# Performance work log

Measured on AMD Instinct MI355X. Metric: run time of the kernel, lower is better.

Reference implementation:

```python
import jax, jax.numpy as jnp
import numpy as np

B, T, C, H, W = 1, 7, 128, 64, 64
IC = C // 2
MB = 256  # codebook size (hardcoded in source)


def setup_inputs() -> dict:
    key = jax.random.key(0)
    ks = jax.random.split(key, 15)
    rn = lambda k, s, sc=1.0: sc * jax.random.normal(k, s, dtype=jnp.float32)
    return {
        "x": rn(ks[0], (B, T, C, H, W)),
        "gn_gamma": 1.0 + rn(ks[1], (C,), 0.1),
        "gn_beta": rn(ks[2], (C,), 0.1),
        "g_w": rn(ks[3], (IC, C), 0.05), "g_b": rn(ks[4], (IC,), 0.05),
        "theta_w": rn(ks[5], (IC, C), 0.05), "theta_b": rn(ks[6], (IC,), 0.05),
        "phi_w": rn(ks[7], (IC, C), 0.05), "phi_b": rn(ks[8], (IC,), 0.05),
        "wz_w": rn(ks[9], (C, IC * 7), 0.05), "wz_b": rn(ks[10], (C,), 0.05),
        "wz1_w": rn(ks[11], (C, IC), 0.05), "wz1_b": rn(ks[12], (C,), 0.05),
        "mb": rn(ks[13], (IC, MB)),
        "std": 4.0 * jnp.ones((1,), jnp.float32),
    }


def _groupnorm(v, gamma, beta, groups=32, eps=1e-6):
    # v: (B_, C_, H_, W_)
    b_ = v.shape[0]
    vr = v.reshape(b_, groups, -1)
    mu = vr.mean(axis=-1, keepdims=True)
    var = vr.var(axis=-1, keepdims=True)
    vn = ((vr - mu) * jax.lax.rsqrt(var + eps)).reshape(v.shape)
    return vn * gamma[:, None, None] + beta[:, None, None]


def _conv1x1(v, w, b):
    # v: (B_, Cin, H, W), w: (Cout, Cin)
    return jnp.einsum('bchw,oc->bohw', v, w) + b[:, None, None]


def reference(x, gn_gamma, gn_beta, g_w, g_b, theta_w, theta_b, phi_w, phi_b,
              wz_w, wz_b, wz1_w, wz1_b, mb, std):
    b, t, c, h, w = x.shape
    ic = g_w.shape[0]
    n = h * w

    # distance matrix D[(i,j),(k,l)] = (j-l)^2 + (i-k)^2  (row-major flatten of (i,j))
    yy, xx = jnp.meshgrid(jnp.arange(h), jnp.arange(w), indexing='ij')
    yf = yy.reshape(-1).astype(x.dtype)
    xf = xx.reshape(-1).astype(x.dtype)
    D = (xf[:, None] - xf[None, :]) ** 2 + (yf[:, None] - yf[None, :]) ** 2  # (n, n)
    weight = jnp.exp(-0.5 * D / (std[0] * std[0]))  # (n, n)

    q = x[:, 3]  # (b, c, h, w)
    hn = _groupnorm(x.reshape(b * t, c, h, w), gn_gamma, gn_beta)
    qn = _groupnorm(q, gn_gamma, gn_beta)

    g_x = _conv1x1(hn, g_w, g_b).reshape(b, t, ic, n)
    theta_x = _conv1x1(hn, theta_w, theta_b).reshape(b, t, ic, n)
    phi = _conv1x1(qn, phi_w, phi_b).reshape(b, ic, n).transpose(0, 2, 1)  # (b, n, ic)

    def frame(_, tg):
        theta_t, g_t = tg  # each (b, ic, n)
        f = jnp.einsum('bnc,bcm->bnm', phi, theta_t)        # (b, n, n)
        fdc = jax.nn.softmax(f, axis=-1) * weight            # post-softmax reweight
        y = jnp.einsum('bnm,bcm->bnc', fdc, g_t)            # (b, n, ic)
        return None, y

    _, ys = jax.lax.scan(frame, None,
                         (theta_x.transpose(1, 0, 2, 3), g_x.transpose(1, 0, 2, 3)))
    # ys: (t, b, n, ic) -> (b, t*ic, h, w)
    corr = ys.transpose(1, 0, 3, 2).reshape(b, t * ic, h, w)
    W_y = _conv1x1(corr, wz_w, wz_b)

    # codebook memory attention
    f1 = jnp.einsum('bnc,ck->bnk', phi, mb) * (float(ic) ** -0.5)
    fdc1 = jax.nn.softmax(f1, axis=-1)
    y1 = jnp.einsum('bnk,ck->bnc', fdc1, mb)  # (b, n, ic)
    qloss = jnp.mean(jnp.abs(phi - y1))
    y1 = y1.transpose(0, 2, 1).reshape(b, ic, h, w)
    W_y1 = _conv1x1(y1, wz1_w, wz1_b)

    z = W_y + q + W_y1
    return z, qloss
```

## Files before the change

kernel.cpp:

```cpp
#include <hip/hip_runtime.h>
#include <hip/hip_bf16.h>

#define TT 7
#define CCH 128
#define ICH 64
#define NHW 4096
#define NSPLIT 4
#define MCHUNK (NHW/NSPLIT)

typedef __attribute__((ext_vector_type(8))) short short8;
typedef __attribute__((ext_vector_type(4))) short sshort4;
typedef __attribute__((ext_vector_type(4))) float floatx4;

#define LOG2E 1.44269504f

static __device__ __forceinline__ short f2bf(float f){
  __hip_bfloat16 h = __float2bfloat16(f);
  return *reinterpret_cast<short*>(&h);
}
static __device__ __forceinline__ float bf2f(short s){
  __hip_bfloat16 h = *reinterpret_cast<__hip_bfloat16*>(&s);
  return __bfloat162float(h);
}

__global__ __launch_bounds__(256) void k_precast(const float* __restrict__ x,
    __hip_bfloat16* __restrict__ xbf, float* __restrict__ sacc, float* __restrict__ s2acc){
  __shared__ short tile[64][66];
  int t = blockIdx.y, n0 = blockIdx.x*64, zh = blockIdx.z;
  int ln = threadIdx.x & 63, w = threadIdx.x >> 6;
  float sl[4] = {0.f,0.f,0.f,0.f}, s2l[4] = {0.f,0.f,0.f,0.f};
  #pragma unroll 4
  for (int ci = 0; ci < 16; ++ci){
    int cl = w*16 + ci;
    float v = x[((size_t)t*CCH + zh*64 + cl)*NHW + n0 + ln];
    tile[ln][cl] = f2bf(v);
    sl[ci>>2]  += v;
    s2l[ci>>2] += v*v;
  }
  #pragma unroll
  for (int off = 32; off; off >>= 1){
    #pragma unroll
    for (int g = 0; g < 4; ++g){
      sl[g]  += __shfl_xor(sl[g],  off);
      s2l[g] += __shfl_xor(s2l[g], off);
    }
  }
  if (ln == 0){
    #pragma unroll
    for (int g = 0; g < 4; ++g){
      atomicAdd(&sacc [t*32 + zh*16 + w*4 + g], sl[g]);
      atomicAdd(&s2acc[t*32 + zh*16 + w*4 + g], s2l[g]);
    }
  }
  __syncthreads();
  int row = threadIdx.x >> 2, seg = threadIdx.x & 3;
  short* dst = reinterpret_cast<short*>(xbf) + ((size_t)t*NHW + n0 + row)*CCH + zh*64 + seg*16;
  #pragma unroll
  for (int k = 0; k < 2; ++k){
    short8 v;
    #pragma unroll
    for (int j = 0; j < 8; ++j) v[j] = tile[row][seg*16 + k*8 + j];
    *reinterpret_cast<short8*>(dst + k*8) = v;
  }
}

__global__ __launch_bounds__(256) void k_setup(
    const float* __restrict__ gw, const float* __restrict__ gb,
    const float* __restrict__ thw, const float* __restrict__ thb,
    const float* __restrict__ phw, const float* __restrict__ phb,
    const float* __restrict__ gamma, const float* __restrict__ beta,
    const float* __restrict__ sacc, const float* __restrict__ s2acc,
    __hip_bfloat16* __restrict__ Wth, float* __restrict__ bth,
    __hip_bfloat16* __restrict__ Wg,  float* __restrict__ bg,
    __hip_bfloat16* __restrict__ Wphi, float* __restrict__ bphi,
    const float* __restrict__ wz, const float* __restrict__ wz1,
    const float* __restrict__ wz_b, const float* __restrict__ wz1_b,
    const float* __restrict__ mb,
    __hip_bfloat16* __restrict__ wzcat, float* __restrict__ biasz,
    __hip_bfloat16* __restrict__ mbT, __hip_bfloat16* __restrict__ mbbf){
  if (blockIdx.x < 240){
    int w = threadIdx.x >> 6, lane = threadIdx.x & 63;
    int oidx = blockIdx.x*4 + w;
    const float *W, *B; __hip_bfloat16 *Wf; float *bfo; int t, o;
    float scale = 1.f;
    if (oidx < 448){ t = oidx >> 6; o = oidx & 63; W = thw; B = thb; Wf = Wth + ((size_t)t*ICH + o)*CCH; bfo = bth + t*64 + o; scale = LOG2E; }
    else if (oidx < 896){ int j = oidx - 448; t = j >> 6; o = j & 63; W = gw; B = gb; Wf = Wg + ((size_t)t*ICH + o)*CCH; bfo = bg + t*64 + o; }
    else { t = 3; o = oidx - 896; W = phw; B = phb; Wf = Wphi + (size_t)o*CCH; bfo = bphi + o; }
    float bp = 0.f;
    #pragma unroll
    for (int h = 0; h < 2; ++h){
      int c = h*64 + lane;
      int g = c >> 2;
      float m  = sacc [t*32+g] * (1.f/16384.f);
      float vr = s2acc[t*32+g] * (1.f/16384.f) - m*m;
      float rs = rsqrtf(vr + 1e-6f);
      float a  = gamma[c]*rs;
      float wv = W[o*CCH + c];
      Wf[c] = __float2bfloat16(wv * a * scale);
      bp += wv * (beta[c] - m*a);
    }
    #pragma unroll
    for (int off = 32; off; off >>= 1) bp += __shfl_xor(bp, off);
    if (lane == 0) *bfo = (bp + B[o]) * scale;
  } else {
    int idx = (blockIdx.x - 240)*256 + threadIdx.x;
    #pragma unroll
    for (int k = 0; k < 2; ++k){
      int i = idx + k*32768;
      int o = i >> 9, kk = i & 511;
      float v = (kk < 448) ? wz[o*448 + kk] : wz1[o*64 + (kk-448)];
      wzcat[i] = __float2bfloat16(v);
    }
    if (idx < 128) biasz[idx] = wz_b[idx] + wz1_b[idx];
    if (idx < 64*256){
      int c = idx >> 8, j = idx & 255;
      float v = mb[idx];
      mbbf[idx] = __float2bfloat16(v);
      mbT[j*64 + c] = __float2bfloat16(v);
    }
  }
}

__global__ __launch_bounds__(256) void k_conv(const __hip_bfloat16* __restrict__ xbf,
    const __hip_bfloat16* __restrict__ Wth, const float* __restrict__ bth,
    const __hip_bfloat16* __restrict__ Wg,  const float* __restrict__ bg,
    const __hip_bfloat16* __restrict__ Wphi, const float* __restrict__ bphi,
    __hip_bfloat16* __restrict__ thetaT, __hip_bfloat16* __restrict__ g_nat,
    __hip_bfloat16* __restrict__ phi_bf){
  const int t = blockIdx.y, n0 = blockIdx.x*64;
  const int w = threadIdx.x >> 6, lane = threadIdx.x & 63;
  const int l15 = lane & 15, quad = lane >> 4;

  const short* xb = reinterpret_cast<const short*>(xbf) + ((size_t)t*NHW + n0)*CCH;
  short8 B[4][4];
  #pragma unroll
  for (int nt = 0; nt < 4; ++nt)
    #pragma unroll
    for (int kk = 0; kk < 4; ++kk)
      B[nt][kk] = *reinterpret_cast<const short8*>(xb + (size_t)(nt*16 + l15)*CCH + kk*32 + quad*8);

  {
    const short* aw = reinterpret_cast<const short*>(Wth) + ((size_t)t*ICH + w*16 + l15)*CCH + quad*8;
    short8 A[4];
    #pragma unroll
    for (int kk = 0; kk < 4; ++kk) A[kk] = *reinterpret_cast<const short8*>(aw + kk*32);
    float4 bv = *reinterpret_cast<const float4*>(bth + t*64 + w*16 + quad*4);
    #pragma unroll
    for (int nt = 0; nt < 4; ++nt){
      floatx4 acc = (floatx4){0.f,0.f,0.f,0.f};
      #pragma unroll
      for (int kk = 0; kk < 4; ++kk) acc = __builtin_amdgcn_mfma_f32_16x16x32_bf16(A[kk], B[nt][kk], acc, 0, 0, 0);
      sshort4 pk;
      pk[0] = f2bf(acc[0] + bv.x); pk[1] = f2bf(acc[1] + bv.y);
      pk[2] = f2bf(acc[2] + bv.z); pk[3] = f2bf(acc[3] + bv.w);
      short* dst = reinterpret_cast<short*>(thetaT) + ((size_t)t*NHW + n0 + nt*16 + l15)*ICH + w*16 + quad*4;
      *reinterpret_cast<sshort4*>(dst) = pk;
    }
  }
  {
    const short* aw = reinterpret_cast<const short*>(Wg) + ((size_t)t*ICH + w*16 + l15)*CCH + quad*8;
    short8 A[4];
    #pragma unroll
    for (int kk = 0; kk < 4; ++kk) A[kk] = *reinterpret_cast<const short8*>(aw + kk*32);
    float4 bv = *reinterpret_cast<const float4*>(bg + t*64 + w*16 + quad*4);
    #pragma unroll
    for (int nt = 0; nt < 4; ++nt){
      floatx4 acc = (floatx4){0.f,0.f,0.f,0.f};
      #pragma unroll
      for (int kk = 0; kk < 4; ++kk) acc = __builtin_amdgcn_mfma_f32_16x16x32_bf16(A[kk], B[nt][kk], acc, 0, 0, 0);
      short* gb = reinterpret_cast<short*>(g_nat);
      float bvv[4] = {bv.x, bv.y, bv.z, bv.w};
      #pragma unroll
      for (int r = 0; r < 4; ++r)
        gb[((size_t)t*ICH + w*16 + quad*4 + r)*NHW + n0 + nt*16 + l15] = f2bf(acc[r] + bvv[r]);
    }
  }
  if (t == 3){
    const short* aw = reinterpret_cast<const short*>(Wphi) + (size_t)(w*16 + l15)*CCH + quad*8;
    short8 A[4];
    #pragma unroll
    for (int kk = 0; kk < 4; ++kk) A[kk] = *reinterpret_cast<const short8*>(aw + kk*32);
    float4 bv = *reinterpret_cast<const float4*>(bphi + w*16 + quad*4);
    #pragma unroll
    for (int nt = 0; nt < 4; ++nt){
      floatx4 acc = (floatx4){0.f,0.f,0.f,0.f};
      #pragma unroll
      for (int kk = 0; kk < 4; ++kk) acc = __builtin_amdgcn_mfma_f32_16x16x32_bf16(A[kk], B[nt][kk], acc, 0, 0, 0);
      sshort4 pk;
      pk[0] = f2bf(acc[0] + bv.x); pk[1] = f2bf(acc[1] + bv.y);
      pk[2] = f2bf(acc[2] + bv.z); pk[3] = f2bf(acc[3] + bv.w);
      short* dst = reinterpret_cast<short*>(phi_bf) + (size_t)(n0 + nt*16 + l15)*ICH + w*16 + quad*4;
      *reinterpret_cast<sshort4*>(dst) = pk;
    }
  }
}

__global__ __launch_bounds__(256, 4) void k_attn(
    const __hip_bfloat16* __restrict__ phi_bf,
    const __hip_bfloat16* __restrict__ thetaT,
    const __hip_bfloat16* __restrict__ g_nat,
    const float* __restrict__ stdp,
    float* __restrict__ Opart, float* __restrict__ Zpart)
{
  const int t    = blockIdx.z;
  const int sp   = blockIdx.y;
  const int w    = threadIdx.x >> 6;
  const int lane = threadIdx.x & 63;
  const int l15  = lane & 15;
  const int quad = lane >> 4;
  const int n0   = blockIdx.x*64;
  const int yn   = blockIdx.x;

  __shared__ short Plds[2][64][72];
  __shared__ float Zsh[4][64];

  const float sstd  = stdp[0];
  const float coefL = -0.5f / (sstd*sstd) * LOG2E;

  const short* phi_s = reinterpret_cast<const short*>(phi_bf);
  const short* th_s  = reinterpret_cast<const short*>(thetaT) + (size_t)t*NHW*ICH;
  const short* g_s   = reinterpret_cast<const short*>(g_nat)  + (size_t)t*ICH*NHW;

  short8 phB[4][2];
  #pragma unroll
  for (int nt = 0; nt < 4; ++nt){
    const short* pp = phi_s + (size_t)(n0 + nt*16 + l15)*ICH + quad*8;
    phB[nt][0] = *reinterpret_cast<const short8*>(pp);
    phB[nt][1] = *reinterpret_cast<const short8*>(pp + 32);
  }

  float wxv[4][4];
  {
    const int xm = w*16 + quad*4;
    #pragma unroll
    for (int nt = 0; nt < 4; ++nt){
      int xn = nt*16 + l15;
      #pragma unroll
      for (int r = 0; r < 4; ++r){
        int dx = xn - (xm + r);
        wxv[nt][r] = exp2f(coefL * (float)(dx*dx));
      }
    }
  }

  const int ci = w >> 1, nj = w & 1;
  floatx4 oacc[2][2];
  #pragma unroll
  for (int a = 0; a < 2; ++a)
    #pragma unroll
    for (int b = 0; b < 2; ++b) oacc[a][b] = (floatx4){0.f,0.f,0.f,0.f};
  float psum[4] = {0.f,0.f,0.f,0.f};

  int m0 = sp*MCHUNK;
  for (int it = 0; it < MCHUNK/64; ++it, m0 += 64){
    const int buf = it & 1;

    short8 gA[2][2];
    #pragma unroll
    for (int ct = 0; ct < 2; ++ct){
      const short* gp = g_s + (size_t)(ci*32 + ct*16 + l15)*NHW + m0 + quad*8;
      gA[ct][0] = *reinterpret_cast<const short8*>(gp);
      gA[ct][1] = *reinterpret_cast<const short8*>(gp + 32);
    }

    const short* tp = th_s + (size_t)(m0 + w*16 + l15)*ICH + quad*8;
    short8 a0 = *reinterpret_cast<const short8*>(tp);
    short8 a1 = *reinterpret_cast<const short8*>(tp + 32);

    floatx4 s[4];
    #pragma unroll
    for (int nt = 0; nt < 4; ++nt){
      floatx4 acc = (floatx4){0.f,0.f,0.f,0.f};
      acc = __builtin_amdgcn_mfma_f32_16x16x32_bf16(a0, phB[nt][0], acc, 0, 0, 0);
      s[nt] = __builtin_amdgcn_mfma_f32_16x16x32_bf16(a1, phB[nt][1], acc, 0, 0, 0);
    }

    const int ym = m0 >> 6;
    const int dy = yn - ym;
    const float wyv = exp2f(coefL * (float)(dy*dy));
    #pragma unroll
    for (int nt = 0; nt < 4; ++nt){
      float pw[4];
      #pragma unroll
      for (int r = 0; r < 4; ++r){
        float p = exp2f(s[nt][r]);
        psum[nt] += p;
        pw[r] = p * (wyv * wxv[nt][r]);
      }
      __hip_bfloat162 lo = __float22bfloat162_rn(make_float2(pw[0], pw[1]));
      __hip_bfloat162 hi = __float22bfloat162_rn(make_float2(pw[2], pw[3]));
      uint2 u;
      u.x = *reinterpret_cast<unsigned*>(&lo);
      u.y = *reinterpret_cast<unsigned*>(&hi);
      *reinterpret_cast<uint2*>(&Plds[buf][nt*16 + l15][w*16 + quad*4]) = u;
    }

    __syncthreads();

    short8 pB[2][2];
    #pragma unroll
    for (int nt2 = 0; nt2 < 2; ++nt2){
      const short* pr = &Plds[buf][nj*32 + nt2*16 + l15][quad*8];
      pB[nt2][0] = *reinterpret_cast<const short8*>(pr);
      pB[nt2][1] = *reinterpret_cast<const short8*>(pr + 32);
    }

    #pragma unroll
    for (int ct = 0; ct < 2; ++ct)
      #pragma unroll
      for (int nt2 = 0; nt2 < 2; ++nt2){
        oacc[ct][nt2] = __builtin_amdgcn_mfma_f32_16x16x32_bf16(gA[ct][0], pB[nt2][0], oacc[ct][nt2], 0, 0, 0);
        oacc[ct][nt2] = __builtin_amdgcn_mfma_f32_16x16x32_bf16(gA[ct][1], pB[nt2][1], oacc[ct][nt2], 0, 0, 0);
      }
  }

  float* Ob = Opart + (size_t)(t*NSPLIT + sp)*ICH*NHW;
  #pragma unroll
  for (int ct = 0; ct < 2; ++ct)
    #pragma unroll
    for (int nt2 = 0; nt2 < 2; ++nt2){
      int c = ci*32 + ct*16 + quad*4;
      int n = n0 + nj*32 + nt2*16 + l15;
      #pragma unroll
      for (int r = 0; r < 4; ++r)
        Ob[(size_t)(c + r)*NHW + n] = oacc[ct][nt2][r];
    }

  #pragma unroll
  for (int nt = 0; nt < 4; ++nt){
    float z = psum[nt];
    z += __shfl_xor(z, 16);
    z += __shfl_xor(z, 32);
    psum[nt] = z;
  }
  if (quad == 0){
    #pragma unroll
    for (int nt = 0; nt < 4; ++nt) Zsh[w][nt*16 + l15] = psum[nt];
  }
  __syncthreads();
  if (threadIdx.x < 64){
    float z = Zsh[0][threadIdx.x] + Zsh[1][threadIdx.x] + Zsh[2][threadIdx.x] + Zsh[3][threadIdx.x];
    Zpart[(size_t)(t*NSPLIT + sp)*NHW + n0 + threadIdx.x] = z;
  }
}

__global__ __launch_bounds__(256) void k_merge(const float* __restrict__ Opart,
    const float* __restrict__ Zpart, __hip_bfloat16* __restrict__ corrT){
  __shared__ short tile[64][72];
  __shared__ float zinv[64];
  const int t = blockIdx.y, n0 = blockIdx.x*64;

  if (threadIdx.x < 64){
    float zs = 0.f;
    #pragma unroll
    for (int s = 0; s < NSPLIT; ++s)
      zs += Zpart[(size_t)(t*NSPLIT + s)*NHW + n0 + threadIdx.x];
    zinv[threadIdx.x] = 1.f / zs;
  }
  __syncthreads();

  const int nq = threadIdx.x & 15, cc = threadIdx.x >> 4;
  #pragma unroll
  for (int cp = 0; cp < 4; ++cp){
    int c = cp*16 + cc;
    float4 acc = {0.f,0.f,0.f,0.f};
    #pragma unroll
    for (int s = 0; s < NSPLIT; ++s){
      float4 v = *reinterpret_cast<const float4*>(
        Opart + ((size_t)(t*NSPLIT + s)*ICH + c)*NHW + n0 + nq*4);
      acc.x += v.x; acc.y += v.y; acc.z += v.z; acc.w += v.w;
    }
    tile[nq*4+0][c] = f2bf(acc.x * zinv[nq*4+0]);
    tile[nq*4+1][c] = f2bf(acc.y * zinv[nq*4+1]);
    tile[nq*4+2][c] = f2bf(acc.z * zinv[nq*4+2]);
    tile[nq*4+3][c] = f2bf(acc.w * zinv[nq*4+3]);
  }
  __syncthreads();

  #pragma unroll
  for (int rep = 0; rep < 2; ++rep){
    int idx = rep*256 + threadIdx.x;
    int n = idx >> 3, seg = idx & 7;
    short8 v = *reinterpret_cast<short8*>(&tile[n][seg*8]);
    *reinterpret_cast<short8*>(reinterpret_cast<short*>(corrT)
        + (size_t)(n0 + n)*512 + t*64 + seg*8) = v;
  }
}

__global__ __launch_bounds__(256) void k_mb(const __hip_bfloat16* __restrict__ phi_bf,
    const __hip_bfloat16* __restrict__ mbT, const __hip_bfloat16* __restrict__ mbbf,
    __hip_bfloat16* __restrict__ corrT, float* __restrict__ qacc){
  const int n0 = blockIdx.x*32;
  const int w = threadIdx.x >> 6, lane = threadIdx.x & 63;
  const int l15 = lane & 15, quad = lane >> 4;

  __shared__ short P[32][264];
  __shared__ float Zsh[4][32];

  const short* phi_s = reinterpret_cast<const short*>(phi_bf);
  const short* mbT_s = reinterpret_cast<const short*>(mbT);
  const short* mb_s  = reinterpret_cast<const short*>(mbbf);

  short8 Bp[2][2];
  #pragma unroll
  for (int nt = 0; nt < 2; ++nt){
    const short* pp = phi_s + (size_t)(n0 + nt*16 + l15)*ICH + quad*8;
    Bp[nt][0] = *reinterpret_cast<const short8*>(pp);
    Bp[nt][1] = *reinterpret_cast<const short8*>(pp + 32);
  }
  float psum[2] = {0.f, 0.f};
  #pragma unroll
  for (int jt = 0; jt < 4; ++jt){
    const short* ap = mbT_s + (size_t)(w*64 + jt*16 + l15)*64 + quad*8;
    short8 A0 = *reinterpret_cast<const short8*>(ap);
    short8 A1 = *reinterpret_cast<const short8*>(ap + 32);
    #pragma unroll
    for (int nt = 0; nt < 2; ++nt){
      floatx4 acc = (floatx4){0.f,0.f,0.f,0.f};
      acc = __builtin_amdgcn_mfma_f32_16x16x32_bf16(A0, Bp[nt][0], acc, 0, 0, 0);
      acc = __builtin_amdgcn_mfma_f32_16x16x32_bf16(A1, Bp[nt][1], acc, 0, 0, 0);
      sshort4 pk;
      #pragma unroll
      for (int r = 0; r < 4; ++r){
        float p = exp2f(acc[r] * (0.125f*LOG2E));
        psum[nt] += p;
        pk[r] = f2bf(p);
      }
      *reinterpret_cast<sshort4*>(&P[nt*16 + l15][w*64 + jt*16 + quad*4]) = pk;
    }
  }
  #pragma unroll
  for (int nt = 0; nt < 2; ++nt){
    float z = psum[nt];
    z += __shfl_xor(z, 16);
    z += __shfl_xor(z, 32);
    if (quad == 0) Zsh[w][nt*16 + l15] = z;
  }
  __syncthreads();

  float ql = 0.f;
  #pragma unroll
  for (int nt = 0; nt < 2; ++nt){
    floatx4 acc = (floatx4){0.f,0.f,0.f,0.f};
    #pragma unroll
    for (int kk = 0; kk < 8; ++kk){
      const short* ap = mb_s + (size_t)(w*16 + l15)*256 + kk*32 + quad*8;
      short8 A = *reinterpret_cast<const short8*>(ap);
      short8 B = *reinterpret_cast<const short8*>(&P[nt*16 + l15][kk*32 + quad*8]);
      acc = __builtin_amdgcn_mfma_f32_16x16x32_bf16(A, B, acc, 0, 0, 0);
    }
    int nn = nt*16 + l15;
    float zt = Zsh[0][nn] + Zsh[1][nn] + Zsh[2][nn] + Zsh[3][nn];
    float rz = 1.f / zt;
    const short* ph = phi_s + (size_t)(n0 + nn)*ICH + w*16 + quad*4;
    sshort4 ph4 = *reinterpret_cast<const sshort4*>(ph);
    sshort4 pk;
    #pragma unroll
    for (int r = 0; r < 4; ++r){
      float y = acc[r] * rz;
      ql += fabsf(bf2f(ph4[r]) - y);
      pk[r] = f2bf(y);
    }
    short* dst = reinterpret_cast<short*>(corrT) + (size_t)(n0 + nn)*512 + 448 + w*16 + quad*4;
    *reinterpret_cast<sshort4*>(dst) = pk;
  }
  #pragma unroll
  for (int off = 32; off; off >>= 1) ql += __shfl_xor(ql, off);
  if (lane == 0) atomicAdd(qacc, ql);
}

__global__ __launch_bounds__(256) void k_z(const __hip_bfloat16* __restrict__ corrT,
    const __hip_bfloat16* __restrict__ wzcat, const float* __restrict__ biasz,
    const float* __restrict__ x, const float* __restrict__ qacc,
    float* __restrict__ out){
  const int n0 = blockIdx.x*16;
  const int w = threadIdx.x >> 6, lane = threadIdx.x & 63;
  const int l15 = lane & 15, quad = lane >> 4;
  const int o0 = blockIdx.y*64 + w*16;

  const short* ct_s = reinterpret_cast<const short*>(corrT) + (size_t)(n0 + l15)*512 + quad*8;
  const short* wz_s = reinterpret_cast<const short*>(wzcat) + (size_t)(o0 + l15)*512 + quad*8;

  floatx4 acc = (floatx4){0.f,0.f,0.f,0.f};
  #pragma unroll
  for (int kk = 0; kk < 16; ++kk){
    short8 A = *reinterpret_cast<const short8*>(wz_s + kk*32);
    short8 B = *reinterpret_cast<const short8*>(ct_s + kk*32);
    acc = __builtin_amdgcn_mfma_f32_16x16x32_bf16(A, B, acc, 0, 0, 0);
  }
  float4 bz = *reinterpret_cast<const float4*>(biasz + o0 + quad*4);
  float bzv[4] = {bz.x, bz.y, bz.z, bz.w};
  #pragma unroll
  for (int r = 0; r < 4; ++r){
    int o = o0 + quad*4 + r;
    int n = n0 + l15;
    float q = x[((size_t)3*CCH + o)*NHW + n];
    out[(size_t)o*NHW + n] = acc[r] + bzv[r] + q;
  }
  if (blockIdx.x == 0 && blockIdx.y == 0 && threadIdx.x == 0)
    out[(size_t)CCH*NHW] = qacc[0] * (1.f/262144.f);
}

extern "C" void kernel_launch(void* const* d_in, const int* in_sizes, int n_in,
                              void* d_out, int out_size, void* d_ws, size_t ws_size,
                              hipStream_t stream){
  const float* x     = (const float*)d_in[0];
  const float* gamma = (const float*)d_in[1];
  const float* beta  = (const float*)d_in[2];
  const float* g_w   = (const float*)d_in[3];
  const float* g_b   = (const float*)d_in[4];
  const float* th_w  = (const float*)d_in[5];
  const float* th_b  = (const float*)d_in[6];
  const float* ph_w  = (const float*)d_in[7];
  const float* ph_b  = (const float*)d_in[8];
  const float* wz_w  = (const float*)d_in[9];
  const float* wz_b  = (const float*)d_in[10];
  const float* wz1_w = (const float*)d_in[11];
  const float* wz1_b = (const float*)d_in[12];
  const float* mb    = (const float*)d_in[13];
  const float* stdp  = (const float*)d_in[14];
  float* out = (float*)d_out;

  char* ws = (char*)d_ws;
  size_t off = 0;
  auto alloc = [&](size_t bytes)->char*{
    char* p = ws + off; off += (bytes + 255) & ~(size_t)255; return p;
  };
  float* zbuf    = (float*)alloc(452*4);
  float* sacc    = zbuf;
  float* s2acc   = zbuf + 224;
  float* qacc    = zbuf + 448;
  __hip_bfloat16* xbf    = (__hip_bfloat16*)alloc((size_t)TT*NHW*CCH*2);
  __hip_bfloat16* Wth    = (__hip_bfloat16*)alloc((size_t)TT*ICH*CCH*2);
  float* bth             = (float*)alloc(TT*64*4);
  __hip_bfloat16* Wg     = (__hip_bfloat16*)alloc((size_t)TT*ICH*CCH*2);
  float* bg              = (float*)alloc(TT*64*4);
  __hip_bfloat16* Wphi   = (__hip_bfloat16*)alloc((size_t)ICH*CCH*2);
  float* bphi            = (float*)alloc(64*4);
  __hip_bfloat16* wzcat  = (__hip_bfloat16*)alloc((size_t)128*512*2);
  float* biasz           = (float*)alloc(128*4);
  __hip_bfloat16* mbT    = (__hip_bfloat16*)alloc((size_t)256*64*2);
  __hip_bfloat16* mbbf   = (__hip_bfloat16*)alloc((size_t)64*256*2);
  __hip_bfloat16* thetaT = (__hip_bfloat16*)alloc((size_t)TT*NHW*ICH*2);
  __hip_bfloat16* g_nat  = (__hip_bfloat16*)alloc((size_t)TT*NHW*ICH*2);
  __hip_bfloat16* phi_bf = (__hip_bfloat16*)alloc((size_t)NHW*ICH*2);
  __hip_bfloat16* corrT  = (__hip_bfloat16*)alloc((size_t)NHW*512*2);
  float* Opart   = (float*)alloc((size_t)TT*NSPLIT*ICH*NHW*4);
  float* Zpart   = (float*)alloc((size_t)TT*NSPLIT*NHW*4);

  hipMemsetAsync(zbuf, 0, 452*4, stream);
  k_precast<<<dim3(64,7,2), 256, 0, stream>>>(x, xbf, sacc, s2acc);
  k_setup<<<368, 256, 0, stream>>>(g_w, g_b, th_w, th_b, ph_w, ph_b, gamma, beta,
                                   sacc, s2acc, Wth, bth, Wg, bg, Wphi, bphi,
                                   wz_w, wz1_w, wz_b, wz1_b, mb, wzcat, biasz, mbT, mbbf);
  k_conv<<<dim3(64,7), 256, 0, stream>>>(xbf, Wth, bth, Wg, bg, Wphi, bphi,
                                         thetaT, g_nat, phi_bf);
  k_attn<<<dim3(64,NSPLIT,7), 256, 0, stream>>>(phi_bf, thetaT, g_nat, stdp, Opart, Zpart);
  k_merge<<<dim3(64,7), 256, 0, stream>>>(Opart, Zpart, corrT);
  k_mb  <<<128, 256, 0, stream>>>(phi_bf, mbT, mbbf, corrT, qacc);
  k_z   <<<dim3(256,2), 256, 0, stream>>>(corrT, wzcat, biasz, x, qacc, out);
}
```

Measured before the change: 247.1 us.

## Drop memset and atomics, split conv into two jobs, merge merge+mb kernels

Group-norm statistics and the qloss sum are now written as per-block partial sums and reduced deterministically by the consumer kernels, replacing the atomics. This also removes the memset launch. The conv kernel gets a z dimension so theta/phi and g projections run in separate blocks, doubling parallelism. The merge and codebook kernels are fused into one launch, and k_attn's launch bounds are raised to 5 waves. Fewer launches and more blocks are traded for serial reduction loops in k_setup and k_z and possible register pressure in k_attn.

```diff
diff --git a/kernel.cpp b/kernel.cpp
--- a/kernel.cpp
+++ b/kernel.cpp
@@ -24,7 +24,7 @@
 }
 
 __global__ __launch_bounds__(256) void k_precast(const float* __restrict__ x,
-    __hip_bfloat16* __restrict__ xbf, float* __restrict__ sacc, float* __restrict__ s2acc){
+    __hip_bfloat16* __restrict__ xbf, float* __restrict__ spart, float* __restrict__ spart2){
   __shared__ short tile[64][66];
   int t = blockIdx.y, n0 = blockIdx.x*64, zh = blockIdx.z;
   int ln = threadIdx.x & 63, w = threadIdx.x >> 6;
@@ -46,11 +46,10 @@
     }
   }
   if (ln == 0){
-    #pragma unroll
-    for (int g = 0; g < 4; ++g){
-      atomicAdd(&sacc [t*32 + zh*16 + w*4 + g], sl[g]);
-      atomicAdd(&s2acc[t*32 + zh*16 + w*4 + g], s2l[g]);
-    }
+    float* sp  = spart  + (size_t)blockIdx.x*224 + t*32 + zh*16 + w*4;
+    float* sp2 = spart2 + (size_t)blockIdx.x*224 + t*32 + zh*16 + w*4;
+    #pragma unroll
+    for (int g = 0; g < 4; ++g){ sp[g] = sl[g]; sp2[g] = s2l[g]; }
   }
   __syncthreads();
   int row = threadIdx.x >> 2, seg = threadIdx.x & 3;
@@ -69,7 +68,7 @@
     const float* __restrict__ thw, const float* __restrict__ thb,
     const float* __restrict__ phw, const float* __restrict__ phb,
     const float* __restrict__ gamma, const float* __restrict__ beta,
-    const float* __restrict__ sacc, const float* __restrict__ s2acc,
+    const float* __restrict__ spart, const float* __restrict__ spart2,
     __hip_bfloat16* __restrict__ Wth, float* __restrict__ bth,
     __hip_bfloat16* __restrict__ Wg,  float* __restrict__ bg,
     __hip_bfloat16* __restrict__ Wphi, float* __restrict__ bphi,
@@ -86,18 +85,28 @@
     if (oidx < 448){ t = oidx >> 6; o = oidx & 63; W = thw; B = thb; Wf = Wth + ((size_t)t*ICH + o)*CCH; bfo = bth + t*64 + o; scale = LOG2E; }
     else if (oidx < 896){ int j = oidx - 448; t = j >> 6; o = j & 63; W = gw; B = gb; Wf = Wg + ((size_t)t*ICH + o)*CCH; bfo = bg + t*64 + o; }
     else { t = 3; o = oidx - 896; W = phw; B = phb; Wf = Wphi + (size_t)o*CCH; bfo = bphi + o; }
+    float mv[2], rv[2];
+    #pragma unroll
+    for (int h = 0; h < 2; ++h){
+      int gid = t*32 + ((h*64 + lane) >> 2);
+      float S = 0.f, S2 = 0.f;
+      for (int i = 0; i < 64; ++i){
+        S  += spart [(size_t)i*224 + gid];
+        S2 += spart2[(size_t)i*224 + gid];
+      }
+      float m  = S * (1.f/16384.f);
+      float vr = S2 * (1.f/16384.f) - m*m;
+      mv[h] = m;
+      rv[h] = rsqrtf(vr + 1e-6f);
+    }
     float bp = 0.f;
     #pragma unroll
     for (int h = 0; h < 2; ++h){
       int c = h*64 + lane;
-      int g = c >> 2;
-      float m  = sacc [t*32+g] * (1.f/16384.f);
-      float vr = s2acc[t*32+g] * (1.f/16384.f) - m*m;
-      float rs = rsqrtf(vr + 1e-6f);
-      float a  = gamma[c]*rs;
+      float a  = gamma[c]*rv[h];
       float wv = W[o*CCH + c];
       Wf[c] = __float2bfloat16(wv * a * scale);
-      bp += wv * (beta[c] - m*a);
+      bp += wv * (beta[c] - mv[h]*a);
     }
     #pragma unroll
     for (int off = 32; off; off >>= 1) bp += __shfl_xor(bp, off);
@@ -127,7 +136,7 @@
     const __hip_bfloat16* __restrict__ Wphi, const float* __restrict__ bphi,
     __hip_bfloat16* __restrict__ thetaT, __hip_bfloat16* __restrict__ g_nat,
     __hip_bfloat16* __restrict__ phi_bf){
-  const int t = blockIdx.y, n0 = blockIdx.x*64;
+  const int t = blockIdx.y, n0 = blockIdx.x*64, job = blockIdx.z;
   const int w = threadIdx.x >> 6, lane = threadIdx.x & 63;
   const int l15 = lane & 15, quad = lane >> 4;
 
@@ -139,25 +148,44 @@
     for (int kk = 0; kk < 4; ++kk)
       B[nt][kk] = *reinterpret_cast<const short8*>(xb + (size_t)(nt*16 + l15)*CCH + kk*32 + quad*8);
 
-  {
-    const short* aw = reinterpret_cast<const short*>(Wth) + ((size_t)t*ICH + w*16 + l15)*CCH + quad*8;
-    short8 A[4];
-    #pragma unroll
-    for (int kk = 0; kk < 4; ++kk) A[kk] = *reinterpret_cast<const short8*>(aw + kk*32);
-    float4 bv = *reinterpret_cast<const float4*>(bth + t*64 + w*16 + quad*4);
-    #pragma unroll
-    for (int nt = 0; nt < 4; ++nt){
-      floatx4 acc = (floatx4){0.f,0.f,0.f,0.f};
-      #pragma unroll
-      for (int kk = 0; kk < 4; ++kk) acc = __builtin_amdgcn_mfma_f32_16x16x32_bf16(A[kk], B[nt][kk], acc, 0, 0, 0);
-      sshort4 pk;
-      pk[0] = f2bf(acc[0] + bv.x); pk[1] = f2bf(acc[1] + bv.y);
-      pk[2] = f2bf(acc[2] + bv.z); pk[3] = f2bf(acc[3] + bv.w);
-      short* dst = reinterpret_cast<short*>(thetaT) + ((size_t)t*NHW + n0 + nt*16 + l15)*ICH + w*16 + quad*4;
-      *reinterpret_cast<sshort4*>(dst) = pk;
-    }
-  }
-  {
+  if (job == 0){
+    {
+      const short* aw = reinterpret_cast<const short*>(Wth) + ((size_t)t*ICH + w*16 + l15)*CCH + quad*8;
+      short8 A[4];
+      #pragma unroll
+      for (int kk = 0; kk < 4; ++kk) A[kk] = *reinterpret_cast<const short8*>(aw + kk*32);
+      float4 bv = *reinterpret_cast<const float4*>(bth + t*64 + w*16 + quad*4);
+      #pragma unroll
+      for (int nt = 0; nt < 4; ++nt){
+        floatx4 acc = (floatx4){0.f,0.f,0.f,0.f};
+        #pragma unroll
+        for (int kk = 0; kk < 4; ++kk) acc = __builtin_amdgcn_mfma_f32_16x16x32_bf16(A[kk], B[nt][kk], acc, 0, 0, 0);
+        sshort4 pk;
+        pk[0] = f2bf(acc[0] + bv.x); pk[1] = f2bf(acc[1] + bv.y);
+        pk[2] = f2bf(acc[2] + bv.z); pk[3] = f2bf(acc[3] + bv.w);
+        short* dst = reinterpret_cast<short*>(thetaT) + ((size_t)t*NHW + n0 + nt*16 + l15)*ICH + w*16 + quad*4;
+        *reinterpret_cast<sshort4*>(dst) = pk;
+      }
+    }
+    if (t == 3){
+      const short* aw = reinterpret_cast<const short*>(Wphi) + (size_t)(w*16 + l15)*CCH + quad*8;
+      short8 A[4];
+      #pragma unroll
+      for (int kk = 0; kk < 4; ++kk) A[kk] = *reinterpret_cast<const short8*>(aw + kk*32);
+      float4 bv = *reinterpret_cast<const float4*>(bphi + w*16 + quad*4);
+      #pragma unroll
+      for (int nt = 0; nt < 4; ++nt){
+        floatx4 acc = (floatx4){0.f,0.f,0.f,0.f};
+        #pragma unroll
+        for (int kk = 0; kk < 4; ++kk) acc = __builtin_amdgcn_mfma_f32_16x16x32_bf16(A[kk], B[nt][kk], acc, 0, 0, 0);
+        sshort4 pk;
+        pk[0] = f2bf(acc[0] + bv.x); pk[1] = f2bf(acc[1] + bv.y);
+        pk[2] = f2bf(acc[2] + bv.z); pk[3] = f2bf(acc[3] + bv.w);
+        short* dst = reinterpret_cast<short*>(phi_bf) + (size_t)(n0 + nt*16 + l15)*ICH + w*16 + quad*4;
+        *reinterpret_cast<sshort4*>(dst) = pk;
+      }
+    }
+  } else {
     const short* aw = reinterpret_cast<const short*>(Wg) + ((size_t)t*ICH + w*16 + l15)*CCH + quad*8;
     short8 A[4];
     #pragma unroll
@@ -175,27 +203,9 @@
         gb[((size_t)t*ICH + w*16 + quad*4 + r)*NHW + n0 + nt*16 + l15] = f2bf(acc[r] + bvv[r]);
     }
   }
-  if (t == 3){
-    const short* aw = reinterpret_cast<const short*>(Wphi) + (size_t)(w*16 + l15)*CCH + quad*8;
-    short8 A[4];
-    #pragma unroll
-    for (int kk = 0; kk < 4; ++kk) A[kk] = *reinterpret_cast<const short8*>(aw + kk*32);
-    float4 bv = *reinterpret_cast<const float4*>(bphi + w*16 + quad*4);
-    #pragma unroll
-    for (int nt = 0; nt < 4; ++nt){
-      floatx4 acc = (floatx4){0.f,0.f,0.f,0.f};
-      #pragma unroll
-      for (int kk = 0; kk < 4; ++kk) acc = __builtin_amdgcn_mfma_f32_16x16x32_bf16(A[kk], B[nt][kk], acc, 0, 0, 0);
-      sshort4 pk;
-      pk[0] = f2bf(acc[0] + bv.x); pk[1] = f2bf(acc[1] + bv.y);
-      pk[2] = f2bf(acc[2] + bv.z); pk[3] = f2bf(acc[3] + bv.w);
-      short* dst = reinterpret_cast<short*>(phi_bf) + (size_t)(n0 + nt*16 + l15)*ICH + w*16 + quad*4;
-      *reinterpret_cast<sshort4*>(dst) = pk;
-    }
-  }
-}
-
-__global__ __launch_bounds__(256, 4) void k_attn(
+}
+
+__global__ __launch_bounds__(256, 5) void k_attn(
     const __hip_bfloat16* __restrict__ phi_bf,
     const __hip_bfloat16* __restrict__ thetaT,
     const __hip_bfloat16* __restrict__ g_nat,
@@ -344,134 +354,140 @@
   }
 }
 
-__global__ __launch_bounds__(256) void k_merge(const float* __restrict__ Opart,
-    const float* __restrict__ Zpart, __hip_bfloat16* __restrict__ corrT){
+__global__ __launch_bounds__(256) void k_post(const float* __restrict__ Opart,
+    const float* __restrict__ Zpart,
+    const __hip_bfloat16* __restrict__ phi_bf,
+    const __hip_bfloat16* __restrict__ mbT, const __hip_bfloat16* __restrict__ mbbf,
+    __hip_bfloat16* __restrict__ corrT, float* __restrict__ qpart){
   __shared__ short tile[64][72];
   __shared__ float zinv[64];
-  const int t = blockIdx.y, n0 = blockIdx.x*64;
-
-  if (threadIdx.x < 64){
-    float zs = 0.f;
-    #pragma unroll
-    for (int s = 0; s < NSPLIT; ++s)
-      zs += Zpart[(size_t)(t*NSPLIT + s)*NHW + n0 + threadIdx.x];
-    zinv[threadIdx.x] = 1.f / zs;
-  }
-  __syncthreads();
-
-  const int nq = threadIdx.x & 15, cc = threadIdx.x >> 4;
-  #pragma unroll
-  for (int cp = 0; cp < 4; ++cp){
-    int c = cp*16 + cc;
-    float4 acc = {0.f,0.f,0.f,0.f};
-    #pragma unroll
-    for (int s = 0; s < NSPLIT; ++s){
-      float4 v = *reinterpret_cast<const float4*>(
-        Opart + ((size_t)(t*NSPLIT + s)*ICH + c)*NHW + n0 + nq*4);
-      acc.x += v.x; acc.y += v.y; acc.z += v.z; acc.w += v.w;
-    }
-    tile[nq*4+0][c] = f2bf(acc.x * zinv[nq*4+0]);
-    tile[nq*4+1][c] = f2bf(acc.y * zinv[nq*4+1]);
-    tile[nq*4+2][c] = f2bf(acc.z * zinv[nq*4+2]);
-    tile[nq*4+3][c] = f2bf(acc.w * zinv[nq*4+3]);
-  }
-  __syncthreads();
-
-  #pragma unroll
-  for (int rep = 0; rep < 2; ++rep){
-    int idx = rep*256 + threadIdx.x;
-    int n = idx >> 3, seg = idx & 7;
-    short8 v = *reinterpret_cast<short8*>(&tile[n][seg*8]);
-    *reinterpret_cast<short8*>(reinterpret_cast<short*>(corrT)
-        + (size_t)(n0 + n)*512 + t*64 + seg*8) = v;
-  }
-}
-
-__global__ __launch_bounds__(256) void k_mb(const __hip_bfloat16* __restrict__ phi_bf,
-    const __hip_bfloat16* __restrict__ mbT, const __hip_bfloat16* __restrict__ mbbf,
-    __hip_bfloat16* __restrict__ corrT, float* __restrict__ qacc){
-  const int n0 = blockIdx.x*32;
-  const int w = threadIdx.x >> 6, lane = threadIdx.x & 63;
-  const int l15 = lane & 15, quad = lane >> 4;
-
   __shared__ short P[32][264];
   __shared__ float Zsh[4][32];
-
-  const short* phi_s = reinterpret_cast<const short*>(phi_bf);
-  const short* mbT_s = reinterpret_cast<const short*>(mbT);
-  const short* mb_s  = reinterpret_cast<const short*>(mbbf);
-
-  short8 Bp[2][2];
-  #pragma unroll
-  for (int nt = 0; nt < 2; ++nt){
-    const short* pp = phi_s + (size_t)(n0 + nt*16 + l15)*ICH + quad*8;
-    Bp[nt][0] = *reinterpret_cast<const short8*>(pp);
-    Bp[nt][1] = *reinterpret_cast<const short8*>(pp + 32);
-  }
-  float psum[2] = {0.f, 0.f};
-  #pragma unroll
-  for (int jt = 0; jt < 4; ++jt){
-    const short* ap = mbT_s + (size_t)(w*64 + jt*16 + l15)*64 + quad*8;
-    short8 A0 = *reinterpret_cast<const short8*>(ap);
-    short8 A1 = *reinterpret_cast<const short8*>(ap + 32);
+  __shared__ float qred[4];
+
+  const int b = blockIdx.x;
+  if (b < 448){
+    const int t = b >> 6, n0 = (b & 63)*64;
+    if (threadIdx.x < 64){
+      float zs = 0.f;
+      #pragma unroll
+      for (int s = 0; s < NSPLIT; ++s)
+        zs += Zpart[(size_t)(t*NSPLIT + s)*NHW + n0 + threadIdx.x];
+      zinv[threadIdx.x] = 1.f / zs;
+    }
+    __syncthreads();
+
+    const int nq = threadIdx.x & 15, cc = threadIdx.x >> 4;
+    #pragma unroll
+    for (int cp = 0; cp < 4; ++cp){
+      int c = cp*16 + cc;
+      float4 acc = {0.f,0.f,0.f,0.f};
+      #pragma unroll
+      for (int s = 0; s < NSPLIT; ++s){
+        float4 v = *reinterpret_cast<const float4*>(
+          Opart + ((size_t)(t*NSPLIT + s)*ICH + c)*NHW + n0 + nq*4);
+        acc.x += v.x; acc.y += v.y; acc.z += v.z; acc.w += v.w;
+      }
+      tile[nq*4+0][c] = f2bf(acc.x * zinv[nq*4+0]);
+      tile[nq*4+1][c] = f2bf(acc.y * zinv[nq*4+1]);
+      tile[nq*4+2][c] = f2bf(acc.z * zinv[nq*4+2]);
+      tile[nq*4+3][c] = f2bf(acc.w * zinv[nq*4+3]);
+    }
+    __syncthreads();
+
+    #pragma unroll
+    for (int rep = 0; rep < 2; ++rep){
+      int idx = rep*256 + threadIdx.x;
+      int n = idx >> 3, seg = idx & 7;
+      short8 v = *reinterpret_cast<short8*>(&tile[n][seg*8]);
+      *reinterpret_cast<short8*>(reinterpret_cast<short*>(corrT)
+          + (size_t)(n0 + n)*512 + t*64 + seg*8) = v;
+    }
+  } else {
+    const int mbid = b - 448;
+    const int n0 = mbid*32;
+    const int w = threadIdx.x >> 6, lane = threadIdx.x & 63;
+    const int l15 = lane & 15, quad = lane >> 4;
+
+    const short* phi_s = reinterpret_cast<const short*>(phi_bf);
+    const short* mbT_s = reinterpret_cast<const short*>(mbT);
+    const short* mb_s  = reinterpret_cast<const short*>(mbbf);
+
+    short8 Bp[2][2];
+    #pragma unroll
+    for (int nt = 0; nt < 2; ++nt){
+      const short* pp = phi_s + (size_t)(n0 + nt*16 + l15)*ICH + quad*8;
+      Bp[nt][0] = *reinterpret_cast<const short8*>(pp);
+      Bp[nt][1] = *reinterpret_cast<const short8*>(pp + 32);
+    }
+    float psum[2] = {0.f, 0.f};
+    #pragma unroll
+    for (int jt = 0; jt < 4; ++jt){
+      const short* ap = mbT_s + (size_t)(w*64 + jt*16 + l15)*64 + quad*8;
+      short8 A0 = *reinterpret_cast<const short8*>(ap);
+      short8 A1 = *reinterpret_cast<const short8*>(ap + 32);
+      #pragma unroll
+      for (int nt = 0; nt < 2; ++nt){
+        floatx4 acc = (floatx4){0.f,0.f,0.f,0.f};
+        acc = __builtin_amdgcn_mfma_f32_16x16x32_bf16(A0, Bp[nt][0], acc, 0, 0, 0);
+        acc = __builtin_amdgcn_mfma_f32_16x16x32_bf16(A1, Bp[nt][1], acc, 0, 0, 0);
+        sshort4 pk;
+        #pragma unroll
+        for (int r = 0; r < 4; ++r){
+          float p = exp2f(acc[r] * (0.125f*LOG2E));
+          psum[nt] += p;
+          pk[r] = f2bf(p);
+        }
+        *reinterpret_cast<sshort4*>(&P[nt*16 + l15][w*64 + jt*16 + quad*4]) = pk;
+      }
+    }
+    #pragma unroll
+    for (int nt = 0; nt < 2; ++nt){
+      float z = psum[nt];
+      z += __shfl_xor(z, 16);
+      z += __shfl_xor(z, 32);
+      if (quad == 0) Zsh[w][nt*16 + l15] = z;
+    }
+    __syncthreads();
+
+    float ql = 0.f;
     #pragma unroll
     for (int nt = 0; nt < 2; ++nt){
       floatx4 acc = (floatx4){0.f,0.f,0.f,0.f};
-      acc = __builtin_amdgcn_mfma_f32_16x16x32_bf16(A0, Bp[nt][0], acc, 0, 0, 0);
-      acc = __builtin_amdgcn_mfma_f32_16x16x32_bf16(A1, Bp[nt][1], acc, 0, 0, 0);
+      #pragma unroll
+      for (int kk = 0; kk < 8; ++kk){
+        const short* ap = mb_s + (size_t)(w*16 + l15)*256 + kk*32 + quad*8;
+        short8 A = *reinterpret_cast<const short8*>(ap);
+        short8 Bv = *reinterpret_cast<const short8*>(&P[nt*16 + l15][kk*32 + quad*8]);
+        acc = __builtin_amdgcn_mfma_f32_16x16x32_bf16(A, Bv, acc, 0, 0, 0);
+      }
+      int nn = nt*16 + l15;
+      float zt = Zsh[0][nn] + Zsh[1][nn] + Zsh[2][nn] + Zsh[3][nn];
+      float rz = 1.f / zt;
+      const short* ph = phi_s + (size_t)(n0 + nn)*ICH + w*16 + quad*4;
+      sshort4 ph4 = *reinterpret_cast<const sshort4*>(ph);
       sshort4 pk;
       #pragma unroll
       for (int r = 0; r < 4; ++r){
-        float p = exp2f(acc[r] * (0.125f*LOG2E));
-        psum[nt] += p;
-        pk[r] = f2bf(p);
-      }
-      *reinterpret_cast<sshort4*>(&P[nt*16 + l15][w*64 + jt*16 + quad*4]) = pk;
-    }
-  }
-  #pragma unroll
-  for (int nt = 0; nt < 2; ++nt){
-    float z = psum[nt];
-    z += __shfl_xor(z, 16);
-    z += __shfl_xor(z, 32);
-    if (quad == 0) Zsh[w][nt*16 + l15] = z;
-  }
-  __syncthreads();
-
-  float ql = 0.f;
-  #pragma unroll
-  for (int nt = 0; nt < 2; ++nt){
-    floatx4 acc = (floatx4){0.f,0.f,0.f,0.f};
-    #pragma unroll
-    for (int kk = 0; kk < 8; ++kk){
-      const short* ap = mb_s + (size_t)(w*16 + l15)*256 + kk*32 + quad*8;
-      short8 A = *reinterpret_cast<const short8*>(ap);
-      short8 B = *reinterpret_cast<const short8*>(&P[nt*16 + l15][kk*32 + quad*8]);
-      acc = __builtin_amdgcn_mfma_f32_16x16x32_bf16(A, B, acc, 0, 0, 0);
-    }
-    int nn = nt*16 + l15;
-    float zt = Zsh[0][nn] + Zsh[1][nn] + Zsh[2][nn] + Zsh[3][nn];
-    float rz = 1.f / zt;
-    const short* ph = phi_s + (size_t)(n0 + nn)*ICH + w*16 + quad*4;
-    sshort4 ph4 = *reinterpret_cast<const sshort4*>(ph);
-    sshort4 pk;
-    #pragma unroll
-    for (int r = 0; r < 4; ++r){
-      float y = acc[r] * rz;
-      ql += fabsf(bf2f(ph4[r]) - y);
-      pk[r] = f2bf(y);
-    }
-    short* dst = reinterpret_cast<short*>(corrT) + (size_t)(n0 + nn)*512 + 448 + w*16 + quad*4;
-    *reinterpret_cast<sshort4*>(dst) = pk;
-  }
-  #pragma unroll
-  for (int off = 32; off; off >>= 1) ql += __shfl_xor(ql, off);
-  if (lane == 0) atomicAdd(qacc, ql);
+        float y = acc[r] * rz;
+        ql += fabsf(bf2f(ph4[r]) - y);
+        pk[r] = f2bf(y);
+      }
+      short* dst = reinterpret_cast<short*>(corrT) + (size_t)(n0 + nn)*512 + 448 + w*16 + quad*4;
+      *reinterpret_cast<sshort4*>(dst) = pk;
+    }
+    #pragma unroll
+    for (int off = 32; off; off >>= 1) ql += __shfl_xor(ql, off);
+    if (lane == 0) qred[w] = ql;
+    __syncthreads();
+    if (threadIdx.x == 0)
+      qpart[mbid] = qred[0] + qred[1] + qred[2] + qred[3];
+  }
 }
 
 __global__ __launch_bounds__(256) void k_z(const __hip_bfloat16* __restrict__ corrT,
     const __hip_bfloat16* __restrict__ wzcat, const float* __restrict__ biasz,
-    const float* __restrict__ x, const float* __restrict__ qacc,
+    const float* __restrict__ x, const float* __restrict__ qpart,
     float* __restrict__ out){
   const int n0 = blockIdx.x*16;
   const int w = threadIdx.x >> 6, lane = threadIdx.x & 63;
@@ -497,8 +513,11 @@
     float q = x[((size_t)3*CCH + o)*NHW + n];
     out[(size_t)o*NHW + n] = acc[r] + bzv[r] + q;
   }
-  if (blockIdx.x == 0 && blockIdx.y == 0 && threadIdx.x == 0)
-    out[(size_t)CCH*NHW] = qacc[0] * (1.f/262144.f);
+  if (blockIdx.x == 0 && blockIdx.y == 0 && threadIdx.x == 0){
+    float s = 0.f;
+    for (int i = 0; i < 128; ++i) s += qpart[i];
+    out[(size_t)CCH*NHW] = s * (1.f/262144.f);
+  }
 }
 
 extern "C" void kernel_launch(void* const* d_in, const int* in_sizes, int n_in,
@@ -526,10 +545,9 @@
   auto alloc = [&](size_t bytes)->char*{
     char* p = ws + off; off += (bytes + 255) & ~(size_t)255; return p;
   };
-  float* zbuf    = (float*)alloc(452*4);
-  float* sacc    = zbuf;
-  float* s2acc   = zbuf + 224;
-  float* qacc    = zbuf + 448;
+  float* spart   = (float*)alloc((size_t)64*224*4);
+  float* spart2  = (float*)alloc((size_t)64*224*4);
+  float* qpart   = (float*)alloc(128*4);
   __hip_bfloat16* xbf    = (__hip_bfloat16*)alloc((size_t)TT*NHW*CCH*2);
   __hip_bfloat16* Wth    = (__hip_bfloat16*)alloc((size_t)TT*ICH*CCH*2);
   float* bth             = (float*)alloc(TT*64*4);
@@ -548,15 +566,13 @@
   float* Opart   = (float*)alloc((size_t)TT*NSPLIT*ICH*NHW*4);
   float* Zpart   = (float*)alloc((size_t)TT*NSPLIT*NHW*4);
 
-  hipMemsetAsync(zbuf, 0, 452*4, stream);
-  k_precast<<<dim3(64,7,2), 256, 0, stream>>>(x, xbf, sacc, s2acc);
+  k_precast<<<dim3(64,7,2), 256, 0, stream>>>(x, xbf, spart, spart2);
   k_setup<<<368, 256, 0, stream>>>(g_w, g_b, th_w, th_b, ph_w, ph_b, gamma, beta,
-                                   sacc, s2acc, Wth, bth, Wg, bg, Wphi, bphi,
+                                   spart, spart2, Wth, bth, Wg, bg, Wphi, bphi,
                                    wz_w, wz1_w, wz_b, wz1_b, mb, wzcat, biasz, mbT, mbbf);
-  k_conv<<<dim3(64,7), 256, 0, stream>>>(xbf, Wth, bth, Wg, bg, Wphi, bphi,
-                                         thetaT, g_nat, phi_bf);
+  k_conv<<<dim3(64,7,2), 256, 0, stream>>>(xbf, Wth, bth, Wg, bg, Wphi, bphi,
+                                           thetaT, g_nat, phi_bf);
   k_attn<<<dim3(64,NSPLIT,7), 256, 0, stream>>>(phi_bf, thetaT, g_nat, stdp, Opart, Zpart);
-  k_merge<<<dim3(64,7), 256, 0, stream>>>(Opart, Zpart, corrT);
-  k_mb  <<<128, 256, 0, stream>>>(phi_bf, mbT, mbbf, corrT, qacc);
-  k_z   <<<dim3(256,2), 256, 0, stream>>>(corrT, wzcat, biasz, x, qacc, out);
-}
+  k_post<<<576, 256, 0, stream>>>(Opart, Zpart, phi_bf, mbT, mbbf, corrT, qpart);
+  k_z   <<<dim3(256,2), 256, 0, stream>>>(corrT, wzcat, biasz, x, qpart, out);
+}
```

After: 267.5 us. 8.3% more time.
